# Performance work log

Measured on AMD Instinct MI355X. Metric: run time of the kernel, lower is better.

The kernel has to match this reference:

```python
import jax, jax.numpy as jnp
import numpy as np

ALPHA_MIN = 1e-6
SN_EPS = 1e-6


def _spectral_normalize(W, u):
    # One power iteration (torch spectral_norm, n_power_iterations=1).
    v = W.T @ u
    v = v / (jnp.linalg.norm(v) + SN_EPS)
    u1 = W @ v
    u1 = u1 / (jnp.linalg.norm(u1) + SN_EPS)
    u1 = jax.lax.stop_gradient(u1)
    v = jax.lax.stop_gradient(v)
    sigma = u1 @ (W @ v)
    return W / sigma


def setup_inputs() -> dict:
    key = jax.random.key(0)
    ks = jax.random.split(key, 11)
    B, T, D, K = 32, 2048, 512, 128
    x = jax.random.normal(ks[0], (B, T, D), jnp.float32)
    dt = jax.random.uniform(ks[1], (B, T), jnp.float32)
    alpha_mod = jax.random.normal(ks[2], (B, T, K), jnp.float32)
    omega_mod = jax.random.normal(ks[3], (B, T, K), jnp.float32)
    tau_mod = jax.random.normal(ks[4], (B, T, 1), jnp.float32)
    s_real_raw = jax.random.normal(ks[5], (K,), jnp.float32)
    s_imag = jax.random.normal(ks[6], (K,), jnp.float32)
    tau_raw = jax.random.normal(ks[7], (1,), jnp.float32)
    W_orig = jax.random.normal(ks[8], (K, D), jnp.float32) * (1.0 / np.sqrt(D))
    b = jax.random.normal(ks[9], (K,), jnp.float32) * 0.01
    u_sn = jax.random.normal(ks[10], (K,), jnp.float32)
    u_sn = u_sn / jnp.linalg.norm(u_sn)
    return {"x": x, "dt": dt, "alpha_mod": alpha_mod, "omega_mod": omega_mod,
            "tau_mod": tau_mod, "s_real_raw": s_real_raw, "s_imag": s_imag,
            "tau_raw": tau_raw, "W_orig": W_orig, "b": b, "u_sn": u_sn}


def reference(x, dt, alpha_mod, omega_mod, tau_mod, s_real_raw, s_imag,
              tau_raw, W_orig, b, u_sn):
    B, T, D = x.shape
    K = W_orig.shape[0]

    # global timescale and poles
    tau = jax.nn.softplus(tau_raw[0]) + 1e-3
    alpha0 = (jax.nn.softplus(s_real_raw) + ALPHA_MIN) * tau  # [K]
    omega0 = s_imag * tau                                      # [K]

    # time-varying modulation (all log-scale)
    scale = jnp.exp(tau_mod)                                   # [B,T,1]
    alpha = alpha0 * jnp.exp(alpha_mod) * scale                # [B,T,K]
    omega = omega0 * jnp.exp(omega_mod) * scale                # [B,T,K]

    dt3 = dt[..., None]                                        # [B,T,1]
    rho = jnp.exp(-alpha * dt3)                                # [B,T,K]
    theta = omega * dt3
    cos_t = jnp.cos(theta)
    sin_t = jnp.sin(theta)

    # spectral-norm projection u = x @ W_sn^T + b -> [B,T,K]
    W_sn = _spectral_normalize(W_orig, u_sn)
    u = jnp.einsum('btd,kd->btk', x, W_sn) + b

    # complex recurrence: z_t = rho_t * e^{i theta_t} * z_{t-1} + u_t
    def step(carry, inp):
        c, s = carry
        rt, ct, st, ut = inp
        c_new = rt * (c * ct - s * st) + ut
        s_new = rt * (c * st + s * ct)
        return (c_new, s_new), (c_new, s_new)

    xs = (jnp.swapaxes(rho, 0, 1), jnp.swapaxes(cos_t, 0, 1),
          jnp.swapaxes(sin_t, 0, 1), jnp.swapaxes(u, 0, 1))  # [T,B,K]
    init = (jnp.zeros((B, K), u.dtype), jnp.zeros((B, K), u.dtype))
    _, (C, S) = jax.lax.scan(step, init, xs)
    C = jnp.swapaxes(C, 0, 1)  # [B,T,K]
    S = jnp.swapaxes(S, 0, 1)
    return jnp.concatenate([C, S], axis=-1)  # [B,T,2K]
```

## Files before the change

kernel.cpp:

```cpp
#include <hip/hip_runtime.h>
#include <hip/hip_bf16.h>
#include <math.h>

typedef __bf16 bf16x8 __attribute__((ext_vector_type(8)));
typedef __bf16 bf16x4 __attribute__((ext_vector_type(4)));
typedef __bf16 bf16x2 __attribute__((ext_vector_type(2)));
typedef float f32x4 __attribute__((ext_vector_type(4)));

#define B_SZ 32
#define T_SZ 2048
#define D_SZ 512
#define K_SZ 128
#define TC 32
#define NC 64

__device__ __forceinline__ float softplus_f(float x){
  return x > 20.f ? x : log1pf(expf(x));
}

__global__ __launch_bounds__(512) void sn_prep(const float* __restrict__ W,
                                               const float* __restrict__ u_sn,
                                               __bf16* __restrict__ Wb){
  __shared__ float red[512];
  __shared__ float vsh[512];
  __shared__ float ush[128];
  const int t = threadIdx.x;
  if (t < 128) ush[t] = u_sn[t];
  __syncthreads();
  float t1 = 0.f;
  #pragma unroll 8
  for (int k = 0; k < K_SZ; ++k) t1 += W[k*D_SZ + t] * ush[k];
  red[t] = t1 * t1;
  __syncthreads();
  for (int s = 256; s > 0; s >>= 1){ if (t < s) red[t] += red[t+s]; __syncthreads(); }
  const float n1 = sqrtf(red[0]);
  vsh[t] = t1 / (n1 + 1e-6f);
  __syncthreads();
  float t2 = 0.f;
  if (t < 128){
    const float4* Wr = (const float4*)(W + (size_t)t * D_SZ);
    const float4* vp = (const float4*)vsh;
    #pragma unroll 8
    for (int d = 0; d < D_SZ/4; ++d){
      const float4 a = Wr[d], v = vp[d];
      t2 += a.x*v.x + a.y*v.y + a.z*v.z + a.w*v.w;
    }
  }
  __syncthreads();
  red[t] = (t < 128) ? t2*t2 : 0.f;
  __syncthreads();
  for (int s = 256; s > 0; s >>= 1){ if (t < s) red[t] += red[t+s]; __syncthreads(); }
  const float n2sq = red[0];
  const float sigma = n2sq / (sqrtf(n2sq) + 1e-6f);
  const float inv = 1.f / sigma;
  for (int i = t; i < K_SZ*D_SZ/4; i += 512){
    const float4 v = ((const float4*)W)[i];
    bf16x4 o; o[0]=(__bf16)(v.x*inv); o[1]=(__bf16)(v.y*inv);
    o[2]=(__bf16)(v.z*inv); o[3]=(__bf16)(v.w*inv);
    ((bf16x4*)Wb)[i] = o;
  }
}

__global__ __launch_bounds__(256) void gemm_xw(const float* __restrict__ X,
                                               const __bf16* __restrict__ Wb,
                                               __bf16* __restrict__ U){
  __shared__ bf16x8 As[2][1024];
  __shared__ bf16x8 Bs[2][1024];
  const int tid = threadIdx.x;
  const int lane = tid & 63;
  const int wid = tid >> 6;
  const int wm = wid >> 1, wn = wid & 1;
  const int rowbase = blockIdx.x * 128;
  const int L15 = lane & 15, Lq = lane >> 4;
  f32x4 acc[4][4] = {};

  const int rowA = tid >> 3;
  const int cg   = tid & 7;
  const int colo = cg * 8;
  int pidx[4];
  #pragma unroll
  for (int r = 0; r < 4; ++r){
    const int row = rowA + 32*r;
    const int fb = ((row >> 4) << 1) | (cg >> 2);
    const int ll = (row & 15) | ((cg & 3) << 4);
    pidx[r] = (fb*64 + ll) ^ cg;
  }
  const float* Xb  = X  + (size_t)(rowbase + rowA)*D_SZ + colo;
  const __bf16* Bb = Wb + (size_t)rowA*D_SZ + colo;

  float4 va[4], vb[4];
  bf16x8 wreg[4];
  #pragma unroll
  for (int r = 0; r < 4; ++r){
    const float4* q = (const float4*)(Xb + (size_t)(32*r)*D_SZ);
    va[r] = q[0]; vb[r] = q[1];
    wreg[r] = *(const bf16x8*)(Bb + (size_t)(32*r)*D_SZ);
  }

  int pb = 0;
  for (int kk = 0; kk < D_SZ; kk += 64){
    #pragma unroll
    for (int r = 0; r < 4; ++r){
      bf16x8 f;
      f[0]=(__bf16)va[r].x; f[1]=(__bf16)va[r].y; f[2]=(__bf16)va[r].z; f[3]=(__bf16)va[r].w;
      f[4]=(__bf16)vb[r].x; f[5]=(__bf16)vb[r].y; f[6]=(__bf16)vb[r].z; f[7]=(__bf16)vb[r].w;
      As[pb][pidx[r]] = f;
      Bs[pb][pidx[r]] = wreg[r];
    }
    __syncthreads();
    if (kk + 64 < D_SZ){
      #pragma unroll
      for (int r = 0; r < 4; ++r){
        const float4* q = (const float4*)(Xb + (size_t)(32*r)*D_SZ + kk + 64);
        va[r] = q[0]; vb[r] = q[1];
        wreg[r] = *(const bf16x8*)(Bb + (size_t)(32*r)*D_SZ + kk + 64);
      }
    }
    #pragma unroll
    for (int s = 0; s < 2; ++s){
      bf16x8 af[4], bfr[4];
      const int swz = (s << 2) | (lane >> 4);
      #pragma unroll
      for (int ii = 0; ii < 4; ++ii){
        const int fb = ((wm*4+ii) << 1) | s;
        af[ii] = As[pb][(fb*64 + lane) ^ swz];
      }
      #pragma unroll
      for (int jj = 0; jj < 4; ++jj){
        const int fb = ((wn*4+jj) << 1) | s;
        bfr[jj] = Bs[pb][(fb*64 + lane) ^ swz];
      }
      #pragma unroll
      for (int ii = 0; ii < 4; ++ii)
        #pragma unroll
        for (int jj = 0; jj < 4; ++jj)
          acc[ii][jj] = __builtin_amdgcn_mfma_f32_16x16x32_bf16(af[ii], bfr[jj], acc[ii][jj], 0, 0, 0);
    }
    pb ^= 1;
  }
  #pragma unroll
  for (int ii = 0; ii < 4; ++ii){
    const int m = rowbase + (wm*4+ii)*16 + (Lq << 2);
    #pragma unroll
    for (int jj = 0; jj < 4; ++jj){
      const int n = (wn*4+jj)*16 + L15;
      #pragma unroll
      for (int r = 0; r < 4; ++r)
        U[(size_t)(m + r)*K_SZ + n] = (__bf16)acc[ii][jj][r];
    }
  }
}

__global__ __launch_bounds__(256) void pass_a(
    const float* __restrict__ alpha_mod, const float* __restrict__ omega_mod,
    const __bf16* __restrict__ Uarr, const float* __restrict__ dt,
    const float* __restrict__ tau_mod, const float* __restrict__ s_real,
    const float* __restrict__ s_imag, const float* __restrict__ tau_raw,
    const float* __restrict__ bvec,
    float2* __restrict__ sumA, float2* __restrict__ sumT,
    float2* __restrict__ Zr, float2* __restrict__ Zi){
  const int t = threadIdx.x;
  const int kh = t & 63;
  const int cl = t >> 6;
  const int b = blockIdx.y;
  const int c = blockIdx.x*4 + cl;
  const int t0 = c * TC;
  __shared__ float sdt[4*TC], ssc[4*TC];
  if (t < 128){
    const int tg = blockIdx.x*4*TC + t;
    sdt[t] = dt[b*T_SZ + tg];
    ssc[t] = __expf(tau_mod[b*T_SZ + tg]);
  }
  __syncthreads();
  const float tau = softplus_f(tau_raw[0]) + 1e-3f;
  const float2 sr = ((const float2*)s_real)[kh];
  const float2 si = ((const float2*)s_imag)[kh];
  const float2 bk = ((const float2*)bvec)[kh];
  const float a0[2] = {(softplus_f(sr.x)+1e-6f)*tau, (softplus_f(sr.y)+1e-6f)*tau};
  const float w0[2] = {si.x*tau, si.y*tau};
  float zr[2]={0,0}, zs[2]={0,0}, sA[2]={0,0}, sT[2]={0,0};
  const float* sd = sdt + cl*TC;
  const float* ss = ssc + cl*TC;
  const size_t row = (size_t)(b*T_SZ + t0);
  const float2* amp = (const float2*)(alpha_mod + row*K_SZ) + kh;
  const float2* omp = (const float2*)(omega_mod + row*K_SZ) + kh;
  const bf16x2* up  = (const bf16x2*)(Uarr + row*K_SZ) + kh;
  #pragma unroll 4
  for (int i = 0; i < TC; ++i){
    const float2 am = amp[(size_t)i*64];
    const float2 om = omp[(size_t)i*64];
    const bf16x2 u2 = up[(size_t)i*64];
    const float scdt = ss[i] * sd[i];
    #pragma unroll
    for (int j = 0; j < 2; ++j){
      const float ad = a0[j] * __expf(j ? am.y : am.x) * scdt;
      const float th = w0[j] * __expf(j ? om.y : om.x) * scdt;
      const float rho = __expf(-ad);
      float st, ct; __sincosf(th, &st, &ct);
      const float uu = (float)u2[j] + (j ? bk.y : bk.x);
      const float nr = rho*(zr[j]*ct - zs[j]*st) + uu;
      const float ns = rho*(zr[j]*st + zs[j]*ct);
      zr[j] = nr; zs[j] = ns;
      sA[j] += ad; sT[j] += th;
    }
  }
  const size_t idx = ((size_t)(b*NC + c))*64 + kh;
  sumA[idx] = make_float2(sA[0], sA[1]);
  sumT[idx] = make_float2(sT[0], sT[1]);
  Zr[idx]   = make_float2(zr[0], zr[1]);
  Zi[idx]   = make_float2(zs[0], zs[1]);
}

__global__ __launch_bounds__(256) void pass_b(
    const float2* __restrict__ sumA, const float2* __restrict__ sumT,
    const float2* __restrict__ Zr, const float2* __restrict__ Zi,
    float2* __restrict__ Cr, float2* __restrict__ Ci){
  const int id = blockIdx.x*256 + threadIdx.x;
  const int b = id >> 6, kh = id & 63;
  float er[2]={0,0}, ei[2]={0,0};
  #pragma unroll 4
  for (int c = 0; c < NC; ++c){
    const size_t idx = ((size_t)(b*NC + c))*64 + kh;
    Cr[idx] = make_float2(er[0], er[1]);
    Ci[idx] = make_float2(ei[0], ei[1]);
    const float2 sa = sumA[idx], st4 = sumT[idx];
    const float2 zr = Zr[idx],   zi  = Zi[idx];
    #pragma unroll
    for (int j = 0; j < 2; ++j){
      const float rho = __expf(-(j ? sa.y : sa.x));
      float st, ct; __sincosf(j ? st4.y : st4.x, &st, &ct);
      const float ar = rho*ct, ai = rho*st;
      const float zrj = j ? zr.y : zr.x, zij = j ? zi.y : zi.x;
      const float nr = zrj + ar*er[j] - ai*ei[j];
      const float ni = zij + ar*ei[j] + ai*er[j];
      er[j] = nr; ei[j] = ni;
    }
  }
}

__global__ __launch_bounds__(256) void pass_c(
    const float* __restrict__ alpha_mod, const float* __restrict__ omega_mod,
    const __bf16* __restrict__ Uarr, const float* __restrict__ dt,
    const float* __restrict__ tau_mod, const float* __restrict__ s_real,
    const float* __restrict__ s_imag, const float* __restrict__ tau_raw,
    const float* __restrict__ bvec,
    const float2* __restrict__ Cr, const float2* __restrict__ Ci,
    float* __restrict__ out){
  const int t = threadIdx.x;
  const int kh = t & 63;
  const int cl = t >> 6;
  const int b = blockIdx.y;
  const int c = blockIdx.x*4 + cl;
  const int t0 = c * TC;
  __shared__ float sdt[4*TC], ssc[4*TC];
  if (t < 128){
    const int tg = blockIdx.x*4*TC + t;
    sdt[t] = dt[b*T_SZ + tg];
    ssc[t] = __expf(tau_mod[b*T_SZ + tg]);
  }
  __syncthreads();
  const float tau = softplus_f(tau_raw[0]) + 1e-3f;
  const float2 sr = ((const float2*)s_real)[kh];
  const float2 si = ((const float2*)s_imag)[kh];
  const float2 bk = ((const float2*)bvec)[kh];
  const float a0[2] = {(softplus_f(sr.x)+1e-6f)*tau, (softplus_f(sr.y)+1e-6f)*tau};
  const float w0[2] = {si.x*tau, si.y*tau};
  const size_t cidx = ((size_t)(b*NC + c))*64 + kh;
  const float2 cr = Cr[cidx], cim = Ci[cidx];
  float zr[2] = {cr.x, cr.y}, zs[2] = {cim.x, cim.y};
  const float* sd = sdt + cl*TC;
  const float* ss = ssc + cl*TC;
  const size_t row = (size_t)(b*T_SZ + t0);
  const float2* amp = (const float2*)(alpha_mod + row*K_SZ) + kh;
  const float2* omp = (const float2*)(omega_mod + row*K_SZ) + kh;
  const bf16x2* up  = (const bf16x2*)(Uarr + row*K_SZ) + kh;
  float2* outC = (float2*)(out + row*(2*K_SZ)) + kh;
  float2* outS = outC + 64;
  #pragma unroll 4
  for (int i = 0; i < TC; ++i){
    const float2 am = amp[(size_t)i*64];
    const float2 om = omp[(size_t)i*64];
    const bf16x2 u2 = up[(size_t)i*64];
    const float scdt = ss[i] * sd[i];
    #pragma unroll
    for (int j = 0; j < 2; ++j){
      const float ad = a0[j] * __expf(j ? am.y : am.x) * scdt;
      const float th = w0[j] * __expf(j ? om.y : om.x) * scdt;
      const float rho = __expf(-ad);
      float st, ct; __sincosf(th, &st, &ct);
      const float uu = (float)u2[j] + (j ? bk.y : bk.x);
      const float nr = rho*(zr[j]*ct - zs[j]*st) + uu;
      const float ns = rho*(zr[j]*st + zs[j]*ct);
      zr[j] = nr; zs[j] = ns;
    }
    outC[(size_t)i*128] = make_float2(zr[0], zr[1]);
    outS[(size_t)i*128] = make_float2(zs[0], zs[1]);
  }
}

extern "C" void kernel_launch(void* const* d_in, const int* in_sizes, int n_in,
                              void* d_out, int out_size, void* d_ws, size_t ws_size,
                              hipStream_t stream){
  (void)in_sizes; (void)n_in; (void)out_size; (void)ws_size;
  const float* x         = (const float*)d_in[0];
  const float* dt        = (const float*)d_in[1];
  const float* alpha_mod = (const float*)d_in[2];
  const float* omega_mod = (const float*)d_in[3];
  const float* tau_mod   = (const float*)d_in[4];
  const float* s_real    = (const float*)d_in[5];
  const float* s_imag    = (const float*)d_in[6];
  const float* tau_raw   = (const float*)d_in[7];
  const float* W         = (const float*)d_in[8];
  const float* bvec      = (const float*)d_in[9];
  const float* u_sn      = (const float*)d_in[10];
  float* out = (float*)d_out;

  char* w = (char*)d_ws;
  __bf16* Wb = (__bf16*)w;
  __bf16* U  = (__bf16*)(w + 131072);
  size_t off = 131072 + (size_t)B_SZ*T_SZ*K_SZ*2;
  const size_t SUMN = (size_t)B_SZ*NC*K_SZ*4;
  float2* sumA = (float2*)(w + off); off += SUMN;
  float2* sumT = (float2*)(w + off); off += SUMN;
  float2* Zr   = (float2*)(w + off); off += SUMN;
  float2* Zi   = (float2*)(w + off); off += SUMN;
  float2* Cr   = (float2*)(w + off); off += SUMN;
  float2* Ci   = (float2*)(w + off); off += SUMN;

  sn_prep<<<1, 512, 0, stream>>>(W, u_sn, Wb);
  gemm_xw<<<(B_SZ*T_SZ)/128, 256, 0, stream>>>(x, Wb, U);
  pass_a<<<dim3(NC/4, B_SZ), 256, 0, stream>>>(alpha_mod, omega_mod, U, dt, tau_mod,
                                               s_real, s_imag, tau_raw, bvec,
                                               sumA, sumT, Zr, Zi);
  pass_b<<<8, 256, 0, stream>>>(sumA, sumT, Zr, Zi, Cr, Ci);
  pass_c<<<dim3(NC/4, B_SZ), 256, 0, stream>>>(alpha_mod, omega_mod, U, dt, tau_mod,
                                               s_real, s_imag, tau_raw, bvec,
                                               Cr, Ci, out);
}
```

Baseline: 333.8 us.

## Drop LDS from projection GEMM, pre-swizzle weights, and halve scan chunk length

The spectral-norm prep kernel now writes the normalized bf16 weights in MFMA fragment order, so the GEMM can load B fragments straight from global/L2 without shared memory or barriers. Each wave now computes a 32x128 output tile with a two-stage register prefetch of X, and the kernel requests 3 blocks per CU. Separately, the chunked scan uses 16-step chunks instead of 32, which doubles the number of chunks and gives more parallel blocks in pass_a and pass_c. pass_b walks a longer serial chain of chunks with a smaller launch, and the GEMM reads W repeatedly from cache.

```diff
diff --git a/kernel.cpp b/kernel.cpp
--- a/kernel.cpp
+++ b/kernel.cpp
@@ -11,8 +11,8 @@
 #define T_SZ 2048
 #define D_SZ 512
 #define K_SZ 128
-#define TC 32
-#define NC 64
+#define TC 16
+#define NC 128
 
 __device__ __forceinline__ float softplus_f(float x){
   return x > 20.f ? x : log1pf(expf(x));
@@ -53,100 +53,75 @@
   const float n2sq = red[0];
   const float sigma = n2sq / (sqrtf(n2sq) + 1e-6f);
   const float inv = 1.f / sigma;
-  for (int i = t; i < K_SZ*D_SZ/4; i += 512){
-    const float4 v = ((const float4*)W)[i];
-    bf16x4 o; o[0]=(__bf16)(v.x*inv); o[1]=(__bf16)(v.y*inv);
-    o[2]=(__bf16)(v.z*inv); o[3]=(__bf16)(v.w*inv);
-    ((bf16x4*)Wb)[i] = o;
-  }
-}
-
-__global__ __launch_bounds__(256) void gemm_xw(const float* __restrict__ X,
-                                               const __bf16* __restrict__ Wb,
-                                               __bf16* __restrict__ U){
-  __shared__ bf16x8 As[2][1024];
-  __shared__ bf16x8 Bs[2][1024];
+  for (int i = t; i < (K_SZ*D_SZ)/8; i += 512){
+    const int ls = i & 63, fr = i >> 6;
+    const int jj = fr & 7,  ks = fr >> 3;
+    const int n = jj*16 + (ls & 15);
+    const int k = ks*32 + ((ls >> 4) << 3);
+    const float4* src = (const float4*)(W + (size_t)n*D_SZ + k);
+    const float4 s0 = src[0], s1 = src[1];
+    bf16x8 o;
+    o[0]=(__bf16)(s0.x*inv); o[1]=(__bf16)(s0.y*inv);
+    o[2]=(__bf16)(s0.z*inv); o[3]=(__bf16)(s0.w*inv);
+    o[4]=(__bf16)(s1.x*inv); o[5]=(__bf16)(s1.y*inv);
+    o[6]=(__bf16)(s1.z*inv); o[7]=(__bf16)(s1.w*inv);
+    ((bf16x8*)Wb)[i] = o;
+  }
+}
+
+__global__ __launch_bounds__(256, 3) void gemm_xw(const float* __restrict__ X,
+                                                  const __bf16* __restrict__ Wf,
+                                                  __bf16* __restrict__ U){
   const int tid = threadIdx.x;
   const int lane = tid & 63;
-  const int wid = tid >> 6;
-  const int wm = wid >> 1, wn = wid & 1;
-  const int rowbase = blockIdx.x * 128;
-  const int L15 = lane & 15, Lq = lane >> 4;
-  f32x4 acc[4][4] = {};
-
-  const int rowA = tid >> 3;
-  const int cg   = tid & 7;
-  const int colo = cg * 8;
-  int pidx[4];
+  const int wid  = tid >> 6;
+  const int rowbase = blockIdx.x*128 + wid*32;
+  const int r16 = lane & 15, kq = lane >> 4;
+  const float* X0 = X + (size_t)(rowbase + r16)*D_SZ + (kq << 3);
+  const float* X1 = X0 + (size_t)16*D_SZ;
+  const bf16x8* Wp = (const bf16x8*)Wf + lane;
+  f32x4 acc[2][8] = {};
+
+  float4 pa[2][4];
   #pragma unroll
-  for (int r = 0; r < 4; ++r){
-    const int row = rowA + 32*r;
-    const int fb = ((row >> 4) << 1) | (cg >> 2);
-    const int ll = (row & 15) | ((cg & 3) << 4);
-    pidx[r] = (fb*64 + ll) ^ cg;
-  }
-  const float* Xb  = X  + (size_t)(rowbase + rowA)*D_SZ + colo;
-  const __bf16* Bb = Wb + (size_t)rowA*D_SZ + colo;
-
-  float4 va[4], vb[4];
-  bf16x8 wreg[4];
+  for (int p = 0; p < 2; ++p){
+    const float4* q0 = (const float4*)(X0 + p*32);
+    const float4* q1 = (const float4*)(X1 + p*32);
+    pa[p][0]=q0[0]; pa[p][1]=q0[1]; pa[p][2]=q1[0]; pa[p][3]=q1[1];
+  }
   #pragma unroll
-  for (int r = 0; r < 4; ++r){
-    const float4* q = (const float4*)(Xb + (size_t)(32*r)*D_SZ);
-    va[r] = q[0]; vb[r] = q[1];
-    wreg[r] = *(const bf16x8*)(Bb + (size_t)(32*r)*D_SZ);
-  }
-
-  int pb = 0;
-  for (int kk = 0; kk < D_SZ; kk += 64){
-    #pragma unroll
-    for (int r = 0; r < 4; ++r){
-      bf16x8 f;
-      f[0]=(__bf16)va[r].x; f[1]=(__bf16)va[r].y; f[2]=(__bf16)va[r].z; f[3]=(__bf16)va[r].w;
-      f[4]=(__bf16)vb[r].x; f[5]=(__bf16)vb[r].y; f[6]=(__bf16)vb[r].z; f[7]=(__bf16)vb[r].w;
-      As[pb][pidx[r]] = f;
-      Bs[pb][pidx[r]] = wreg[r];
-    }
-    __syncthreads();
-    if (kk + 64 < D_SZ){
-      #pragma unroll
-      for (int r = 0; r < 4; ++r){
-        const float4* q = (const float4*)(Xb + (size_t)(32*r)*D_SZ + kk + 64);
-        va[r] = q[0]; vb[r] = q[1];
-        wreg[r] = *(const bf16x8*)(Bb + (size_t)(32*r)*D_SZ + kk + 64);
-      }
-    }
-    #pragma unroll
-    for (int s = 0; s < 2; ++s){
-      bf16x8 af[4], bfr[4];
-      const int swz = (s << 2) | (lane >> 4);
-      #pragma unroll
-      for (int ii = 0; ii < 4; ++ii){
-        const int fb = ((wm*4+ii) << 1) | s;
-        af[ii] = As[pb][(fb*64 + lane) ^ swz];
-      }
-      #pragma unroll
-      for (int jj = 0; jj < 4; ++jj){
-        const int fb = ((wn*4+jj) << 1) | s;
-        bfr[jj] = Bs[pb][(fb*64 + lane) ^ swz];
-      }
-      #pragma unroll
-      for (int ii = 0; ii < 4; ++ii)
-        #pragma unroll
-        for (int jj = 0; jj < 4; ++jj)
-          acc[ii][jj] = __builtin_amdgcn_mfma_f32_16x16x32_bf16(af[ii], bfr[jj], acc[ii][jj], 0, 0, 0);
-    }
-    pb ^= 1;
+  for (int ks = 0; ks < 16; ++ks){
+    const int cur = ks & 1;
+    bf16x8 a0, a1;
+    {
+      const float4 u0 = pa[cur][0], u1 = pa[cur][1];
+      a0[0]=(__bf16)u0.x; a0[1]=(__bf16)u0.y; a0[2]=(__bf16)u0.z; a0[3]=(__bf16)u0.w;
+      a0[4]=(__bf16)u1.x; a0[5]=(__bf16)u1.y; a0[6]=(__bf16)u1.z; a0[7]=(__bf16)u1.w;
+      const float4 u2 = pa[cur][2], u3 = pa[cur][3];
+      a1[0]=(__bf16)u2.x; a1[1]=(__bf16)u2.y; a1[2]=(__bf16)u2.z; a1[3]=(__bf16)u2.w;
+      a1[4]=(__bf16)u3.x; a1[5]=(__bf16)u3.y; a1[6]=(__bf16)u3.z; a1[7]=(__bf16)u3.w;
+    }
+    if (ks + 2 < 16){
+      const float4* q0 = (const float4*)(X0 + (ks+2)*32);
+      const float4* q1 = (const float4*)(X1 + (ks+2)*32);
+      pa[cur][0]=q0[0]; pa[cur][1]=q0[1]; pa[cur][2]=q1[0]; pa[cur][3]=q1[1];
+    }
+    #pragma unroll
+    for (int jj = 0; jj < 8; ++jj){
+      const bf16x8 bv = Wp[(ks*8 + jj)*64];
+      acc[0][jj] = __builtin_amdgcn_mfma_f32_16x16x32_bf16(a0, bv, acc[0][jj], 0, 0, 0);
+      acc[1][jj] = __builtin_amdgcn_mfma_f32_16x16x32_bf16(a1, bv, acc[1][jj], 0, 0, 0);
+    }
   }
   #pragma unroll
-  for (int ii = 0; ii < 4; ++ii){
-    const int m = rowbase + (wm*4+ii)*16 + (Lq << 2);
-    #pragma unroll
-    for (int jj = 0; jj < 4; ++jj){
-      const int n = (wn*4+jj)*16 + L15;
+  for (int ii = 0; ii < 2; ++ii){
+    const int m0 = rowbase + ii*16 + (kq << 2);
+    #pragma unroll
+    for (int jj = 0; jj < 8; ++jj){
+      const int n = jj*16 + r16;
       #pragma unroll
       for (int r = 0; r < 4; ++r)
-        U[(size_t)(m + r)*K_SZ + n] = (__bf16)acc[ii][jj][r];
+        U[(size_t)(m0 + r)*K_SZ + n] = (__bf16)acc[ii][jj][r];
     }
   }
 }
@@ -166,7 +141,7 @@
   const int c = blockIdx.x*4 + cl;
   const int t0 = c * TC;
   __shared__ float sdt[4*TC], ssc[4*TC];
-  if (t < 128){
+  if (t < 4*TC){
     const int tg = blockIdx.x*4*TC + t;
     sdt[t] = dt[b*T_SZ + tg];
     ssc[t] = __expf(tau_mod[b*T_SZ + tg]);
@@ -185,7 +160,7 @@
   const float2* amp = (const float2*)(alpha_mod + row*K_SZ) + kh;
   const float2* omp = (const float2*)(omega_mod + row*K_SZ) + kh;
   const bf16x2* up  = (const bf16x2*)(Uarr + row*K_SZ) + kh;
-  #pragma unroll 4
+  #pragma unroll 8
   for (int i = 0; i < TC; ++i){
     const float2 am = amp[(size_t)i*64];
     const float2 om = omp[(size_t)i*64];
@@ -211,14 +186,13 @@
   Zi[idx]   = make_float2(zs[0], zs[1]);
 }
 
-__global__ __launch_bounds__(256) void pass_b(
+__global__ __launch_bounds__(64) void pass_b(
     const float2* __restrict__ sumA, const float2* __restrict__ sumT,
     const float2* __restrict__ Zr, const float2* __restrict__ Zi,
     float2* __restrict__ Cr, float2* __restrict__ Ci){
-  const int id = blockIdx.x*256 + threadIdx.x;
-  const int b = id >> 6, kh = id & 63;
+  const int b = blockIdx.x, kh = threadIdx.x;
   float er[2]={0,0}, ei[2]={0,0};
-  #pragma unroll 4
+  #pragma unroll 8
   for (int c = 0; c < NC; ++c){
     const size_t idx = ((size_t)(b*NC + c))*64 + kh;
     Cr[idx] = make_float2(er[0], er[1]);
@@ -253,7 +227,7 @@
   const int c = blockIdx.x*4 + cl;
   const int t0 = c * TC;
   __shared__ float sdt[4*TC], ssc[4*TC];
-  if (t < 128){
+  if (t < 4*TC){
     const int tg = blockIdx.x*4*TC + t;
     sdt[t] = dt[b*T_SZ + tg];
     ssc[t] = __expf(tau_mod[b*T_SZ + tg]);
@@ -276,7 +250,7 @@
   const bf16x2* up  = (const bf16x2*)(Uarr + row*K_SZ) + kh;
   float2* outC = (float2*)(out + row*(2*K_SZ)) + kh;
   float2* outS = outC + 64;
-  #pragma unroll 4
+  #pragma unroll 8
   for (int i = 0; i < TC; ++i){
     const float2 am = amp[(size_t)i*64];
     const float2 om = omp[(size_t)i*64];
@@ -332,7 +306,7 @@
   pass_a<<<dim3(NC/4, B_SZ), 256, 0, stream>>>(alpha_mod, omega_mod, U, dt, tau_mod,
                                                s_real, s_imag, tau_raw, bvec,
                                                sumA, sumT, Zr, Zi);
-  pass_b<<<8, 256, 0, stream>>>(sumA, sumT, Zr, Zi, Cr, Ci);
+  pass_b<<<B_SZ, 64, 0, stream>>>(sumA, sumT, Zr, Zi, Cr, Ci);
   pass_c<<<dim3(NC/4, B_SZ), 256, 0, stream>>>(alpha_mod, omega_mod, U, dt, tau_mod,
                                                s_real, s_imag, tau_raw, bvec,
                                                Cr, Ci, out);
```

After: 420.2 us. 25.9% more time.
